# Kernel optimization log

Measured on AMD Instinct MI355X. Metric: run time of the kernel, lower is better.

Reference implementation:

```python
import jax, jax.numpy as jnp
import numpy as np

N_NODES = 50000
N_EDGES = 800000
F_IN = 128
HID = 128
N_CLASSES = 16
N_GRAPHS = 64


def _glorot(key, shape):
    fan_in, fan_out = shape[0], shape[1]
    lim = (6.0 / (fan_in + fan_out)) ** 0.5
    return jax.random.uniform(key, shape, jnp.float32, -lim, lim)


def setup_inputs() -> dict:
    key = jax.random.key(0)
    ks = jax.random.split(key, 12)
    x = jax.random.normal(ks[0], (N_NODES, F_IN), jnp.float32)
    edge_index = jax.random.randint(ks[1], (2, N_EDGES), 0, N_NODES, jnp.int64)
    batch = jnp.sort(jax.random.randint(ks[2], (N_NODES,), 0, N_GRAPHS, jnp.int64))
    W0 = _glorot(ks[3], (F_IN, HID)); b0 = jnp.zeros((HID,), jnp.float32)
    W1 = _glorot(ks[4], (HID, HID)); b1 = jnp.zeros((HID,), jnp.float32)
    W2 = _glorot(ks[5], (HID, HID)); b2 = jnp.zeros((HID,), jnp.float32)
    Wc = _glorot(ks[6], (HID, N_CLASSES)); bc = jnp.zeros((N_CLASSES,), jnp.float32)
    return {"x": x, "edge_index": edge_index, "batch": batch,
            "W0": W0, "b0": b0, "W1": W1, "b1": b1, "W2": W2, "b2": b2,
            "Wc": Wc, "bc": bc}


def _gcn_prep(edge_index, n_nodes):
    # add self-loops, compute symmetric normalization coefficients
    loop = jnp.arange(n_nodes, dtype=edge_index.dtype)
    src = jnp.concatenate([edge_index[0], loop])
    dst = jnp.concatenate([edge_index[1], loop])
    deg = jax.ops.segment_sum(jnp.ones_like(dst, jnp.float32), dst, num_segments=n_nodes)
    dinv = deg ** -0.5  # deg >= 1 due to self-loops
    norm = dinv[src] * dinv[dst]  # [E+N]
    return src, dst, norm


def _gcn_layer(h, W, b, src, dst, norm, n_nodes):
    h = h @ W                                   # [N, out]
    msg = h[src] * norm[:, None]                # gather + scale [E+N, out]
    out = jax.ops.segment_sum(msg, dst, num_segments=n_nodes)  # scatter-add
    return out + b


def reference(x, edge_index, batch, W0, b0, W1, b1, W2, b2, Wc, bc):
    n = x.shape[0]
    src, dst, norm = _gcn_prep(edge_index, n)
    h = _gcn_layer(x, W0, b0, src, dst, norm, n)
    h = jax.nn.relu(h)  # dropout is identity in eval mode
    h = _gcn_layer(h, W1, b1, src, dst, norm, n)
    h = jax.nn.relu(h)
    h = _gcn_layer(h, W2, b2, src, dst, norm, n)
    # scatter-mean pooling over batch ids
    sums = jax.ops.segment_sum(h, batch, num_segments=N_GRAPHS)        # [G, HID]
    cnts = jax.ops.segment_sum(jnp.ones((n,), jnp.float32), batch, num_segments=N_GRAPHS)
    pooled = sums / jnp.maximum(cnts, 1.0)[:, None]
    return pooled @ Wc + bc  # [G, N_CLASSES]
```

## Files before the change

### kernel.cpp

```cpp
#include <hip/hip_runtime.h>
#include <hip/hip_bf16.h>
#include <hip/hip_fp16.h>

#define HID 128
#define NCLS 16
#define NGRAPH 64
#define CHUNK 1024

using bf16x8 = __attribute__((ext_vector_type(8))) short;
using f32x4  = __attribute__((ext_vector_type(4))) float;

__device__ __forceinline__ unsigned int f2bf(float f) {
    unsigned int u = __float_as_uint(f);
    return (u + 0x7FFFu + ((u >> 16) & 1u)) >> 16;
}
__device__ __forceinline__ float bf2f_lo(unsigned int u) { return __uint_as_float(u << 16); }
__device__ __forceinline__ float bf2f_hi(unsigned int u) { return __uint_as_float(u & 0xFFFF0000u); }

__global__ __launch_bounds__(256) void k_init(int* counts, float* pooled, float* cnt, int n) {
    int i = blockIdx.x * 256 + threadIdx.x;
    if (i < n) counts[i] = 0;
    if (i < NGRAPH * HID) pooled[i] = 0.0f;
    if (i < NGRAPH) cnt[i] = 0.0f;
}

__global__ __launch_bounds__(256) void k_hist(const int* __restrict__ dst,
                                              int* counts, int* rank, int e) {
    int i = blockIdx.x * 256 + threadIdx.x;
    if (i < e) rank[i] = atomicAdd(&counts[dst[i]], 1);
}

__global__ __launch_bounds__(256) void k_dinv(const int* __restrict__ counts,
                                              float* dinv, int n) {
    int i = blockIdx.x * 256 + threadIdx.x;
    if (i < n) dinv[i] = rsqrtf((float)(counts[i] + 1));
}

__global__ __launch_bounds__(256) void k_chunksum(const int* __restrict__ counts,
                                                  int* csum, int n) {
    __shared__ int sdata[256];
    int b = blockIdx.x, t = threadIdx.x;
    int base = b * CHUNK + t * 4;
    int s = 0;
    #pragma unroll
    for (int j = 0; j < 4; ++j) { int i = base + j; if (i < n) s += counts[i]; }
    sdata[t] = s; __syncthreads();
    for (int off = 128; off > 0; off >>= 1) {
        if (t < off) sdata[t] += sdata[t + off];
        __syncthreads();
    }
    if (t == 0) csum[b] = sdata[0];
}

__global__ void k_scanchunks(const int* __restrict__ csum, int* coff, int nb) {
    if (blockIdx.x == 0 && threadIdx.x == 0) {
        int run = 0;
        for (int b = 0; b < nb; ++b) { coff[b] = run; run += csum[b]; }
    }
}

__global__ __launch_bounds__(256) void k_rowptr(const int* __restrict__ counts,
                                                const int* __restrict__ coff,
                                                int* rowptr, int n, int e) {
    __shared__ int sincl[256];
    int b = blockIdx.x, t = threadIdx.x;
    int base = b * CHUNK + t * 4;
    int v[4]; int s = 0;
    #pragma unroll
    for (int j = 0; j < 4; ++j) { int i = base + j; v[j] = (i < n) ? counts[i] : 0; s += v[j]; }
    sincl[t] = s; __syncthreads();
    for (int off = 1; off < 256; off <<= 1) {
        int x = sincl[t];
        int y = (t >= off) ? sincl[t - off] : 0;
        __syncthreads();
        sincl[t] = x + y;
        __syncthreads();
    }
    int run = coff[b] + sincl[t] - s;
    #pragma unroll
    for (int j = 0; j < 4; ++j) {
        int i = base + j;
        if (i < n) { rowptr[i] = run; run += v[j]; }
    }
    if (b == 0 && t == 0) rowptr[n] = e;
}

__global__ __launch_bounds__(256) void k_fill(const int* __restrict__ src,
                                              const int* __restrict__ dst,
                                              const int* __restrict__ rank,
                                              const float* __restrict__ dinv,
                                              const int* __restrict__ rowptr,
                                              unsigned int* __restrict__ epk, int e) {
    int i = blockIdx.x * 256 + threadIdx.x;
    if (i >= e) return;
    int s = src[i], d = dst[i];
    int pos = rowptr[d] + rank[i];
    __half h = __float2half(dinv[s] * dinv[d]);
    unsigned int hu = (unsigned int)__half_as_ushort(h);
    epk[pos] = (unsigned int)s | (hu << 16);
}

__global__ __launch_bounds__(256) void k_wprep(const float* __restrict__ W0,
                                               const float* __restrict__ W1,
                                               const float* __restrict__ W2,
                                               unsigned short* __restrict__ Wt) {
    int tid = blockIdx.x * 256 + threadIdx.x;
    if (tid >= 3 * HID * HID) return;
    int m = tid >> 14;
    int r = tid & 16383;
    int c = r >> 7, k = r & 127;
    const float* W = (m == 0) ? W0 : (m == 1) ? W1 : W2;
    Wt[tid] = (unsigned short)f2bf(W[k * HID + c]);
}

__global__ __launch_bounds__(256) void k_gemm_f32(const float* __restrict__ H,
                                                  const unsigned short* __restrict__ Wt,
                                                  unsigned short* __restrict__ Tb16, int n) {
    __shared__ char ldsA[64 * 256];
    int t = threadIdx.x;
    int cg = t & 31;
    int rg = t >> 5;
    int row0 = blockIdx.x * 64;

    #pragma unroll
    for (int i = 0; i < 8; ++i) {
        int lr = rg + i * 8;
        int r = row0 + lr;
        float4 v = make_float4(0.f, 0.f, 0.f, 0.f);
        if (r < n) v = ((const float4*)H)[(size_t)r * 32 + cg];
        uint2 pk;
        pk.x = f2bf(v.x) | (f2bf(v.y) << 16);
        pk.y = f2bf(v.z) | (f2bf(v.w) << 16);
        int byte = lr * 256 + cg * 8;
        *(uint2*)(ldsA + (byte ^ ((lr & 7) << 4))) = pk;
    }
    __syncthreads();

    int lane = t & 63;
    int w = t >> 6;
    int rsub = lane & 15;
    int kg = lane >> 4;
    int rowIdx = w * 16 + rsub;
    int abase = rowIdx * 256 + kg * 16;
    int aswz = (rowIdx & 7) << 4;

    f32x4 acc[8];
    #pragma unroll
    for (int nt = 0; nt < 8; ++nt) acc[nt] = (f32x4)(0.f);

    #pragma unroll
    for (int kk = 0; kk < 4; ++kk) {
        bf16x8 a = *(const bf16x8*)(ldsA + ((abase + kk * 64) ^ aswz));
        int k0 = kk * 32 + kg * 8;
        #pragma unroll
        for (int nt = 0; nt < 8; ++nt) {
            int col = nt * 16 + rsub;
            bf16x8 b = *(const bf16x8*)(Wt + col * 128 + k0);
            acc[nt] = __builtin_amdgcn_mfma_f32_16x16x32_bf16(a, b, acc[nt], 0, 0, 0);
        }
    }

    #pragma unroll
    for (int nt = 0; nt < 8; ++nt) {
        #pragma unroll
        for (int j = 0; j < 4; ++j) {
            int row = row0 + w * 16 + kg * 4 + j;
            int col = nt * 16 + rsub;
            if (row < n) Tb16[(size_t)row * 128 + col] = (unsigned short)f2bf(acc[nt][j]);
        }
    }
}

__global__ __launch_bounds__(256) void k_gemm_bf16(const unsigned short* __restrict__ Hb,
                                                   const unsigned short* __restrict__ Wt,
                                                   unsigned short* __restrict__ Tb16, int n) {
    __shared__ char ldsA[64 * 256];
    int t = threadIdx.x;
    int row0 = blockIdx.x * 64;
    int c16 = t & 15;
    int rbase = t >> 4;

    #pragma unroll
    for (int i = 0; i < 4; ++i) {
        int lr = rbase + i * 16;
        int r = row0 + lr;
        uint4 v = make_uint4(0u, 0u, 0u, 0u);
        if (r < n) v = *(const uint4*)(Hb + (size_t)r * 128 + c16 * 8);
        int byte = lr * 256 + c16 * 16;
        *(uint4*)(ldsA + (byte ^ ((lr & 7) << 4))) = v;
    }
    __syncthreads();

    int lane = t & 63;
    int w = t >> 6;
    int rsub = lane & 15;
    int kg = lane >> 4;
    int rowIdx = w * 16 + rsub;
    int abase = rowIdx * 256 + kg * 16;
    int aswz = (rowIdx & 7) << 4;

    f32x4 acc[8];
    #pragma unroll
    for (int nt = 0; nt < 8; ++nt) acc[nt] = (f32x4)(0.f);

    #pragma unroll
    for (int kk = 0; kk < 4; ++kk) {
        bf16x8 a = *(const bf16x8*)(ldsA + ((abase + kk * 64) ^ aswz));
        int k0 = kk * 32 + kg * 8;
        #pragma unroll
        for (int nt = 0; nt < 8; ++nt) {
            int col = nt * 16 + rsub;
            bf16x8 b = *(const bf16x8*)(Wt + col * 128 + k0);
            acc[nt] = __builtin_amdgcn_mfma_f32_16x16x32_bf16(a, b, acc[nt], 0, 0, 0);
        }
    }

    #pragma unroll
    for (int nt = 0; nt < 8; ++nt) {
        #pragma unroll
        for (int j = 0; j < 4; ++j) {
            int row = row0 + w * 16 + kg * 4 + j;
            int col = nt * 16 + rsub;
            if (row < n) Tb16[(size_t)row * 128 + col] = (unsigned short)f2bf(acc[nt][j]);
        }
    }
}

__global__ __launch_bounds__(256) void k_agg(const unsigned int* __restrict__ Tb,
                                             unsigned int* __restrict__ outB,
                                             float* __restrict__ outF,
                                             const int* __restrict__ rowptr,
                                             const unsigned int* __restrict__ epk,
                                             const float* __restrict__ dinv,
                                             const float* __restrict__ bias,
                                             int n, int mode) {
    int wid = (blockIdx.x * 256 + threadIdx.x) >> 6;
    int lane = threadIdx.x & 63;
    if (wid >= n) return;
    float di = dinv[wid];
    float2 b2 = ((const float2*)bias)[lane];
    unsigned int us = Tb[(size_t)wid * 64 + lane];
    float sn = di * di;
    float2 acc;
    acc.x = fmaf(bf2f_lo(us), sn, b2.x);
    acc.y = fmaf(bf2f_hi(us), sn, b2.y);
    int start = rowptr[wid];
    int deg = rowptr[wid + 1] - start;

    for (int j0 = 0; j0 < deg; j0 += 64) {
        int myj = j0 + lane;
        unsigned int rec = 0;
        if (myj < deg) rec = epk[start + myj];
        int m = min(64, deg - j0);
        int jj = 0;
        for (; jj + 16 <= m; jj += 16) {
            unsigned int rr[16], uu[16];
            #pragma unroll
            for (int k = 0; k < 16; ++k) rr[k] = (unsigned int)__shfl((int)rec, jj + k);
            #pragma unroll
            for (int k = 0; k < 16; ++k) uu[k] = Tb[(size_t)(rr[k] & 0xFFFFu) * 64 + lane];
            #pragma unroll
            for (int k = 0; k < 16; ++k) {
                float wk = __half2float(__ushort_as_half((unsigned short)(rr[k] >> 16)));
                acc.x = fmaf(wk, bf2f_lo(uu[k]), acc.x);
                acc.y = fmaf(wk, bf2f_hi(uu[k]), acc.y);
            }
        }
        for (; jj + 4 <= m; jj += 4) {
            unsigned int rr[4], uu[4];
            #pragma unroll
            for (int k = 0; k < 4; ++k) rr[k] = (unsigned int)__shfl((int)rec, jj + k);
            #pragma unroll
            for (int k = 0; k < 4; ++k) uu[k] = Tb[(size_t)(rr[k] & 0xFFFFu) * 64 + lane];
            #pragma unroll
            for (int k = 0; k < 4; ++k) {
                float wk = __half2float(__ushort_as_half((unsigned short)(rr[k] >> 16)));
                acc.x = fmaf(wk, bf2f_lo(uu[k]), acc.x);
                acc.y = fmaf(wk, bf2f_hi(uu[k]), acc.y);
            }
        }
        for (; jj < m; ++jj) {
            unsigned int rj = (unsigned int)__shfl((int)rec, jj);
            unsigned int u = Tb[(size_t)(rj & 0xFFFFu) * 64 + lane];
            float wj = __half2float(__ushort_as_half((unsigned short)(rj >> 16)));
            acc.x = fmaf(wj, bf2f_lo(u), acc.x);
            acc.y = fmaf(wj, bf2f_hi(u), acc.y);
        }
    }

    if (mode == 0) {
        float rx = fmaxf(acc.x, 0.f), ry = fmaxf(acc.y, 0.f);
        outB[(size_t)wid * 64 + lane] = f2bf(rx) | (f2bf(ry) << 16);
    } else {
        ((float2*)outF)[(size_t)wid * 64 + lane] = acc;
    }
}

__global__ __launch_bounds__(256) void k_pool(const float* __restrict__ H,
                                              const int* __restrict__ batch,
                                              float* pooled, float* cnt, int n) {
    int gw = (blockIdx.x * 256 + threadIdx.x) >> 6;
    int lane = threadIdx.x & 63;
    int n0 = gw * 32;
    if (n0 >= n) return;
    int n1 = min(n0 + 32, n);
    const float2* H2 = (const float2*)H;
    int gprev = batch[n0];
    float2 acc = make_float2(0.f, 0.f);
    float runc = 0.f;
    for (int i = n0; i < n1; ++i) {
        int g = batch[i];
        if (g != gprev) {
            atomicAdd(&pooled[gprev * HID + 2 * lane], acc.x);
            atomicAdd(&pooled[gprev * HID + 2 * lane + 1], acc.y);
            if (lane == 0) atomicAdd(&cnt[gprev], runc);
            acc = make_float2(0.f, 0.f); runc = 0.f; gprev = g;
        }
        float2 v = H2[(size_t)i * 64 + lane];
        acc.x += v.x; acc.y += v.y; runc += 1.f;
    }
    atomicAdd(&pooled[gprev * HID + 2 * lane], acc.x);
    atomicAdd(&pooled[gprev * HID + 2 * lane + 1], acc.y);
    if (lane == 0) atomicAdd(&cnt[gprev], runc);
}

__global__ __launch_bounds__(256) void k_head(const float* __restrict__ pooled,
                                              const float* __restrict__ cnt,
                                              const float* __restrict__ Wc,
                                              const float* __restrict__ bc,
                                              float* __restrict__ out) {
    int idx = blockIdx.x * 256 + threadIdx.x;
    if (idx >= NGRAPH * NCLS) return;
    int g = idx >> 4, c = idx & 15;
    float inv = 1.0f / fmaxf(cnt[g], 1.0f);
    float s = 0.f;
    for (int k = 0; k < HID; ++k)
        s = fmaf(pooled[g * HID + k], Wc[k * NCLS + c], s);
    out[idx] = s * inv + bc[c];
}

extern "C" void kernel_launch(void* const* d_in, const int* in_sizes, int n_in,
                              void* d_out, int out_size, void* d_ws, size_t ws_size,
                              hipStream_t stream) {
    const float* x    = (const float*)d_in[0];
    const int*   ei   = (const int*)d_in[1];
    const int*   batch= (const int*)d_in[2];
    const float* W0   = (const float*)d_in[3];
    const float* b0   = (const float*)d_in[4];
    const float* W1   = (const float*)d_in[5];
    const float* b1   = (const float*)d_in[6];
    const float* W2   = (const float*)d_in[7];
    const float* b2   = (const float*)d_in[8];
    const float* Wc   = (const float*)d_in[9];
    const float* bc   = (const float*)d_in[10];
    float* out = (float*)d_out;

    const int N = in_sizes[0] / HID;
    const int E = in_sizes[1] / 2;
    const int* src = ei;
    const int* dst = ei + E;

    char* p = (char*)d_ws;
    auto alloc = [&](size_t bytes) { void* r = (void*)p; p += (bytes + 255) & ~(size_t)255; return r; };
    int*   counts = (int*)alloc((size_t)N * 4);
    float* dinv   = (float*)alloc((size_t)N * 4);
    int*   rank   = (int*)alloc((size_t)E * 4);
    int*   csum   = (int*)alloc(256 * 4);
    int*   coff   = (int*)alloc(256 * 4);
    int*   rowptr = (int*)alloc((size_t)(N + 1) * 4);
    unsigned int* epk = (unsigned int*)alloc((size_t)E * 4);
    float* pooled = (float*)alloc((size_t)NGRAPH * HID * 4);
    float* cnt    = (float*)alloc((size_t)NGRAPH * 4);
    unsigned short* Tb16 = (unsigned short*)alloc((size_t)N * HID * 2);
    unsigned short* Hb16 = (unsigned short*)alloc((size_t)N * HID * 2);
    float* bufF   = (float*)alloc((size_t)N * HID * 4);
    unsigned short* Wt = (unsigned short*)alloc((size_t)3 * HID * HID * 2);

    const int NB = (N + CHUNK - 1) / CHUNK;

    k_init<<<(N + 255) / 256, 256, 0, stream>>>(counts, pooled, cnt, N);
    k_hist<<<(E + 255) / 256, 256, 0, stream>>>(dst, counts, rank, E);
    k_dinv<<<(N + 255) / 256, 256, 0, stream>>>(counts, dinv, N);
    k_chunksum<<<NB, 256, 0, stream>>>(counts, csum, N);
    k_scanchunks<<<1, 64, 0, stream>>>(csum, coff, NB);
    k_rowptr<<<NB, 256, 0, stream>>>(counts, coff, rowptr, N, E);
    k_fill<<<(E + 255) / 256, 256, 0, stream>>>(src, dst, rank, dinv, rowptr, epk, E);
    k_wprep<<<(3 * HID * HID + 255) / 256, 256, 0, stream>>>(W0, W1, W2, Wt);

    const int gemm_grid = (N + 63) / 64;
    const int agg_grid  = ((size_t)N * 64 + 255) / 256;

    k_gemm_f32<<<gemm_grid, 256, 0, stream>>>(x, Wt, Tb16, N);
    k_agg<<<agg_grid, 256, 0, stream>>>((const unsigned int*)Tb16, (unsigned int*)Hb16, nullptr,
                                        rowptr, epk, dinv, b0, N, 0);
    k_gemm_bf16<<<gemm_grid, 256, 0, stream>>>(Hb16, Wt + 16384, Tb16, N);
    k_agg<<<agg_grid, 256, 0, stream>>>((const unsigned int*)Tb16, (unsigned int*)Hb16, nullptr,
                                        rowptr, epk, dinv, b1, N, 0);
    k_gemm_bf16<<<gemm_grid, 256, 0, stream>>>(Hb16, Wt + 32768, Tb16, N);
    k_agg<<<agg_grid, 256, 0, stream>>>((const unsigned int*)Tb16, nullptr, bufF,
                                        rowptr, epk, dinv, b2, N, 1);

    const int pool_waves = (N + 31) / 32;
    k_pool<<<(pool_waves * 64 + 255) / 256, 256, 0, stream>>>(bufF, batch, pooled, cnt, N);
    k_head<<<(NGRAPH * NCLS + 255) / 256, 256, 0, stream>>>(pooled, cnt, Wc, bc, out);
}
```

Measured before the change: 264.5 us.

## Split feature tables into column halves for cache-resident aggregation; fold prep kernels

The bf16 feature tables are now stored as two 64-column halves. Aggregation runs as two passes per layer, each touching a 6.4 MB half table, so the gathered working set is more likely to stay in L2 or last-level cache. Within each pass a wave splits its edges between two 32-lane groups and reduces them with a cross-half shuffle. The dinv, scan-chunks and weight-prep kernels are folded into init, rowptr and fill, removing several launches. In exchange the edge list and rowptr are read twice per layer, and each aggregation launch does less work per node.

```diff
diff --git a/kernel.cpp b/kernel.cpp
--- a/kernel.cpp
+++ b/kernel.cpp
@@ -17,23 +17,28 @@
 __device__ __forceinline__ float bf2f_lo(unsigned int u) { return __uint_as_float(u << 16); }
 __device__ __forceinline__ float bf2f_hi(unsigned int u) { return __uint_as_float(u & 0xFFFF0000u); }
 
-__global__ __launch_bounds__(256) void k_init(int* counts, float* pooled, float* cnt, int n) {
+__global__ __launch_bounds__(256) void k_init(int* counts, float* pooled, float* cnt,
+                                              const float* __restrict__ W0,
+                                              const float* __restrict__ W1,
+                                              const float* __restrict__ W2,
+                                              unsigned short* __restrict__ Wt, int n) {
     int i = blockIdx.x * 256 + threadIdx.x;
     if (i < n) counts[i] = 0;
     if (i < NGRAPH * HID) pooled[i] = 0.0f;
     if (i < NGRAPH) cnt[i] = 0.0f;
+    if (i < 3 * HID * HID) {
+        int m = i >> 14;
+        int r = i & 16383;
+        int c = r >> 7, k = r & 127;
+        const float* W = (m == 0) ? W0 : (m == 1) ? W1 : W2;
+        Wt[i] = (unsigned short)f2bf(W[k * HID + c]);
+    }
 }
 
 __global__ __launch_bounds__(256) void k_hist(const int* __restrict__ dst,
                                               int* counts, int* rank, int e) {
     int i = blockIdx.x * 256 + threadIdx.x;
     if (i < e) rank[i] = atomicAdd(&counts[dst[i]], 1);
-}
-
-__global__ __launch_bounds__(256) void k_dinv(const int* __restrict__ counts,
-                                              float* dinv, int n) {
-    int i = blockIdx.x * 256 + threadIdx.x;
-    if (i < n) dinv[i] = rsqrtf((float)(counts[i] + 1));
 }
 
 __global__ __launch_bounds__(256) void k_chunksum(const int* __restrict__ counts,
@@ -52,18 +57,18 @@
     if (t == 0) csum[b] = sdata[0];
 }
 
-__global__ void k_scanchunks(const int* __restrict__ csum, int* coff, int nb) {
-    if (blockIdx.x == 0 && threadIdx.x == 0) {
-        int run = 0;
-        for (int b = 0; b < nb; ++b) { coff[b] = run; run += csum[b]; }
-    }
-}
-
 __global__ __launch_bounds__(256) void k_rowptr(const int* __restrict__ counts,
-                                                const int* __restrict__ coff,
+                                                const int* __restrict__ csum,
                                                 int* rowptr, int n, int e) {
     __shared__ int sincl[256];
+    __shared__ int s_coff;
     int b = blockIdx.x, t = threadIdx.x;
+    if (t < 64) {
+        int v = (t < b) ? csum[t] : 0;
+        #pragma unroll
+        for (int off = 32; off > 0; off >>= 1) v += __shfl_xor(v, off);
+        if (t == 0) s_coff = v;
+    }
     int base = b * CHUNK + t * 4;
     int v[4]; int s = 0;
     #pragma unroll
@@ -76,7 +81,7 @@
         sincl[t] = x + y;
         __syncthreads();
     }
-    int run = coff[b] + sincl[t] - s;
+    int run = s_coff + sincl[t] - s;
     #pragma unroll
     for (int j = 0; j < 4; ++j) {
         int i = base + j;
@@ -88,34 +93,23 @@
 __global__ __launch_bounds__(256) void k_fill(const int* __restrict__ src,
                                               const int* __restrict__ dst,
                                               const int* __restrict__ rank,
-                                              const float* __restrict__ dinv,
+                                              const int* __restrict__ counts,
                                               const int* __restrict__ rowptr,
                                               unsigned int* __restrict__ epk, int e) {
     int i = blockIdx.x * 256 + threadIdx.x;
     if (i >= e) return;
     int s = src[i], d = dst[i];
     int pos = rowptr[d] + rank[i];
-    __half h = __float2half(dinv[s] * dinv[d]);
+    float norm = rsqrtf((float)(counts[s] + 1)) * rsqrtf((float)(counts[d] + 1));
+    __half h = __float2half(norm);
     unsigned int hu = (unsigned int)__half_as_ushort(h);
     epk[pos] = (unsigned int)s | (hu << 16);
 }
 
-__global__ __launch_bounds__(256) void k_wprep(const float* __restrict__ W0,
-                                               const float* __restrict__ W1,
-                                               const float* __restrict__ W2,
-                                               unsigned short* __restrict__ Wt) {
-    int tid = blockIdx.x * 256 + threadIdx.x;
-    if (tid >= 3 * HID * HID) return;
-    int m = tid >> 14;
-    int r = tid & 16383;
-    int c = r >> 7, k = r & 127;
-    const float* W = (m == 0) ? W0 : (m == 1) ? W1 : W2;
-    Wt[tid] = (unsigned short)f2bf(W[k * HID + c]);
-}
-
 __global__ __launch_bounds__(256) void k_gemm_f32(const float* __restrict__ H,
                                                   const unsigned short* __restrict__ Wt,
-                                                  unsigned short* __restrict__ Tb16, int n) {
+                                                  unsigned short* __restrict__ Tlo,
+                                                  unsigned short* __restrict__ Thi, int n) {
     __shared__ char ldsA[64 * 256];
     int t = threadIdx.x;
     int cg = t & 31;
@@ -162,18 +156,21 @@
 
     #pragma unroll
     for (int nt = 0; nt < 8; ++nt) {
+        unsigned short* Tb = (nt < 4) ? Tlo : Thi;
         #pragma unroll
         for (int j = 0; j < 4; ++j) {
             int row = row0 + w * 16 + kg * 4 + j;
-            int col = nt * 16 + rsub;
-            if (row < n) Tb16[(size_t)row * 128 + col] = (unsigned short)f2bf(acc[nt][j]);
-        }
-    }
-}
-
-__global__ __launch_bounds__(256) void k_gemm_bf16(const unsigned short* __restrict__ Hb,
+            int col = (nt * 16 + rsub) & 63;
+            if (row < n) Tb[(size_t)row * 64 + col] = (unsigned short)f2bf(acc[nt][j]);
+        }
+    }
+}
+
+__global__ __launch_bounds__(256) void k_gemm_bf16(const unsigned short* __restrict__ Hlo,
+                                                   const unsigned short* __restrict__ Hhi,
                                                    const unsigned short* __restrict__ Wt,
-                                                   unsigned short* __restrict__ Tb16, int n) {
+                                                   unsigned short* __restrict__ Tlo,
+                                                   unsigned short* __restrict__ Thi, int n) {
     __shared__ char ldsA[64 * 256];
     int t = threadIdx.x;
     int row0 = blockIdx.x * 64;
@@ -184,8 +181,9 @@
     for (int i = 0; i < 4; ++i) {
         int lr = rbase + i * 16;
         int r = row0 + lr;
+        const unsigned short* Hb = (c16 < 8) ? Hlo : Hhi;
         uint4 v = make_uint4(0u, 0u, 0u, 0u);
-        if (r < n) v = *(const uint4*)(Hb + (size_t)r * 128 + c16 * 8);
+        if (r < n) v = *(const uint4*)(Hb + (size_t)r * 64 + (c16 & 7) * 8);
         int byte = lr * 256 + c16 * 16;
         *(uint4*)(ldsA + (byte ^ ((lr & 7) << 4))) = v;
     }
@@ -217,82 +215,80 @@
 
     #pragma unroll
     for (int nt = 0; nt < 8; ++nt) {
+        unsigned short* Tb = (nt < 4) ? Tlo : Thi;
         #pragma unroll
         for (int j = 0; j < 4; ++j) {
             int row = row0 + w * 16 + kg * 4 + j;
-            int col = nt * 16 + rsub;
-            if (row < n) Tb16[(size_t)row * 128 + col] = (unsigned short)f2bf(acc[nt][j]);
-        }
-    }
-}
-
-__global__ __launch_bounds__(256) void k_agg(const unsigned int* __restrict__ Tb,
-                                             unsigned int* __restrict__ outB,
-                                             float* __restrict__ outF,
-                                             const int* __restrict__ rowptr,
-                                             const unsigned int* __restrict__ epk,
-                                             const float* __restrict__ dinv,
-                                             const float* __restrict__ bias,
-                                             int n, int mode) {
+            int col = (nt * 16 + rsub) & 63;
+            if (row < n) Tb[(size_t)row * 64 + col] = (unsigned short)f2bf(acc[nt][j]);
+        }
+    }
+}
+
+__global__ __launch_bounds__(256) void k_agg_h(const unsigned int* __restrict__ TbH,
+                                               unsigned int* __restrict__ outB,
+                                               float* __restrict__ outF,
+                                               const int* __restrict__ rowptr,
+                                               const unsigned int* __restrict__ epk,
+                                               const float* __restrict__ biasH,
+                                               int n, int mode, int hoff) {
     int wid = (blockIdx.x * 256 + threadIdx.x) >> 6;
     int lane = threadIdx.x & 63;
     if (wid >= n) return;
-    float di = dinv[wid];
-    float2 b2 = ((const float2*)bias)[lane];
-    unsigned int us = Tb[(size_t)wid * 64 + lane];
-    float sn = di * di;
-    float2 acc;
-    acc.x = fmaf(bf2f_lo(us), sn, b2.x);
-    acc.y = fmaf(bf2f_hi(us), sn, b2.y);
+    int p = lane & 31;
+    int g = lane >> 5;
     int start = rowptr[wid];
     int deg = rowptr[wid + 1] - start;
 
+    float2 acc = make_float2(0.f, 0.f);
+    if (g == 0) {
+        float sn = 1.0f / (float)(deg + 1);
+        unsigned int us = TbH[(size_t)wid * 32 + p];
+        float2 b2 = ((const float2*)biasH)[p];
+        acc.x = fmaf(bf2f_lo(us), sn, b2.x);
+        acc.y = fmaf(bf2f_hi(us), sn, b2.y);
+    }
+
+    int gbase = g * 32;
     for (int j0 = 0; j0 < deg; j0 += 64) {
-        int myj = j0 + lane;
+        int myj = j0 + 2 * p + g;
         unsigned int rec = 0;
         if (myj < deg) rec = epk[start + myj];
-        int m = min(64, deg - j0);
+        int rem = deg - j0 - g;
+        int mg = min(32, (rem + 1) >> 1);
         int jj = 0;
-        for (; jj + 16 <= m; jj += 16) {
-            unsigned int rr[16], uu[16];
+        for (; jj + 8 <= mg; jj += 8) {
+            unsigned int rr[8], uu[8];
             #pragma unroll
-            for (int k = 0; k < 16; ++k) rr[k] = (unsigned int)__shfl((int)rec, jj + k);
+            for (int k = 0; k < 8; ++k) rr[k] = (unsigned int)__shfl((int)rec, gbase + jj + k);
             #pragma unroll
-            for (int k = 0; k < 16; ++k) uu[k] = Tb[(size_t)(rr[k] & 0xFFFFu) * 64 + lane];
+            for (int k = 0; k < 8; ++k) uu[k] = TbH[(size_t)(rr[k] & 0xFFFFu) * 32 + p];
             #pragma unroll
-            for (int k = 0; k < 16; ++k) {
+            for (int k = 0; k < 8; ++k) {
                 float wk = __half2float(__ushort_as_half((unsigned short)(rr[k] >> 16)));
                 acc.x = fmaf(wk, bf2f_lo(uu[k]), acc.x);
                 acc.y = fmaf(wk, bf2f_hi(uu[k]), acc.y);
             }
         }
-        for (; jj + 4 <= m; jj += 4) {
-            unsigned int rr[4], uu[4];
-            #pragma unroll
-            for (int k = 0; k < 4; ++k) rr[k] = (unsigned int)__shfl((int)rec, jj + k);
-            #pragma unroll
-            for (int k = 0; k < 4; ++k) uu[k] = Tb[(size_t)(rr[k] & 0xFFFFu) * 64 + lane];
-            #pragma unroll
-            for (int k = 0; k < 4; ++k) {
-                float wk = __half2float(__ushort_as_half((unsigned short)(rr[k] >> 16)));
-                acc.x = fmaf(wk, bf2f_lo(uu[k]), acc.x);
-                acc.y = fmaf(wk, bf2f_hi(uu[k]), acc.y);
-            }
-        }
-        for (; jj < m; ++jj) {
-            unsigned int rj = (unsigned int)__shfl((int)rec, jj);
-            unsigned int u = Tb[(size_t)(rj & 0xFFFFu) * 64 + lane];
+        for (; jj < mg; ++jj) {
+            unsigned int rj = (unsigned int)__shfl((int)rec, gbase + jj);
+            unsigned int u = TbH[(size_t)(rj & 0xFFFFu) * 32 + p];
             float wj = __half2float(__ushort_as_half((unsigned short)(rj >> 16)));
             acc.x = fmaf(wj, bf2f_lo(u), acc.x);
             acc.y = fmaf(wj, bf2f_hi(u), acc.y);
         }
     }
 
-    if (mode == 0) {
-        float rx = fmaxf(acc.x, 0.f), ry = fmaxf(acc.y, 0.f);
-        outB[(size_t)wid * 64 + lane] = f2bf(rx) | (f2bf(ry) << 16);
-    } else {
-        ((float2*)outF)[(size_t)wid * 64 + lane] = acc;
+    acc.x += __shfl_xor(acc.x, 32);
+    acc.y += __shfl_xor(acc.y, 32);
+
+    if (g == 0) {
+        if (mode == 0) {
+            float rx = fmaxf(acc.x, 0.f), ry = fmaxf(acc.y, 0.f);
+            outB[(size_t)wid * 32 + p] = f2bf(rx) | (f2bf(ry) << 16);
+        } else {
+            ((float2*)outF)[(size_t)wid * 64 + hoff + p] = acc;
+        }
     }
 }
 
@@ -363,42 +359,45 @@
     char* p = (char*)d_ws;
     auto alloc = [&](size_t bytes) { void* r = (void*)p; p += (bytes + 255) & ~(size_t)255; return r; };
     int*   counts = (int*)alloc((size_t)N * 4);
-    float* dinv   = (float*)alloc((size_t)N * 4);
     int*   rank   = (int*)alloc((size_t)E * 4);
     int*   csum   = (int*)alloc(256 * 4);
-    int*   coff   = (int*)alloc(256 * 4);
     int*   rowptr = (int*)alloc((size_t)(N + 1) * 4);
     unsigned int* epk = (unsigned int*)alloc((size_t)E * 4);
     float* pooled = (float*)alloc((size_t)NGRAPH * HID * 4);
     float* cnt    = (float*)alloc((size_t)NGRAPH * 4);
-    unsigned short* Tb16 = (unsigned short*)alloc((size_t)N * HID * 2);
-    unsigned short* Hb16 = (unsigned short*)alloc((size_t)N * HID * 2);
+    unsigned short* Tlo = (unsigned short*)alloc((size_t)N * 64 * 2);
+    unsigned short* Thi = (unsigned short*)alloc((size_t)N * 64 * 2);
+    unsigned short* Hlo = (unsigned short*)alloc((size_t)N * 64 * 2);
+    unsigned short* Hhi = (unsigned short*)alloc((size_t)N * 64 * 2);
     float* bufF   = (float*)alloc((size_t)N * HID * 4);
     unsigned short* Wt = (unsigned short*)alloc((size_t)3 * HID * HID * 2);
 
     const int NB = (N + CHUNK - 1) / CHUNK;
 
-    k_init<<<(N + 255) / 256, 256, 0, stream>>>(counts, pooled, cnt, N);
+    k_init<<<(N + 255) / 256, 256, 0, stream>>>(counts, pooled, cnt, W0, W1, W2, Wt, N);
     k_hist<<<(E + 255) / 256, 256, 0, stream>>>(dst, counts, rank, E);
-    k_dinv<<<(N + 255) / 256, 256, 0, stream>>>(counts, dinv, N);
     k_chunksum<<<NB, 256, 0, stream>>>(counts, csum, N);
-    k_scanchunks<<<1, 64, 0, stream>>>(csum, coff, NB);
-    k_rowptr<<<NB, 256, 0, stream>>>(counts, coff, rowptr, N, E);
-    k_fill<<<(E + 255) / 256, 256, 0, stream>>>(src, dst, rank, dinv, rowptr, epk, E);
-    k_wprep<<<(3 * HID * HID + 255) / 256, 256, 0, stream>>>(W0, W1, W2, Wt);
+    k_rowptr<<<NB, 256, 0, stream>>>(counts, csum, rowptr, N, E);
+    k_fill<<<(E + 255) / 256, 256, 0, stream>>>(src, dst, rank, counts, rowptr, epk, E);
 
     const int gemm_grid = (N + 63) / 64;
     const int agg_grid  = ((size_t)N * 64 + 255) / 256;
 
-    k_gemm_f32<<<gemm_grid, 256, 0, stream>>>(x, Wt, Tb16, N);
-    k_agg<<<agg_grid, 256, 0, stream>>>((const unsigned int*)Tb16, (unsigned int*)Hb16, nullptr,
-                                        rowptr, epk, dinv, b0, N, 0);
-    k_gemm_bf16<<<gemm_grid, 256, 0, stream>>>(Hb16, Wt + 16384, Tb16, N);
-    k_agg<<<agg_grid, 256, 0, stream>>>((const unsigned int*)Tb16, (unsigned int*)Hb16, nullptr,
-                                        rowptr, epk, dinv, b1, N, 0);
-    k_gemm_bf16<<<gemm_grid, 256, 0, stream>>>(Hb16, Wt + 32768, Tb16, N);
-    k_agg<<<agg_grid, 256, 0, stream>>>((const unsigned int*)Tb16, nullptr, bufF,
-                                        rowptr, epk, dinv, b2, N, 1);
+    k_gemm_f32<<<gemm_grid, 256, 0, stream>>>(x, Wt, Tlo, Thi, N);
+    k_agg_h<<<agg_grid, 256, 0, stream>>>((const unsigned int*)Tlo, (unsigned int*)Hlo, nullptr,
+                                          rowptr, epk, b0, N, 0, 0);
+    k_agg_h<<<agg_grid, 256, 0, stream>>>((const unsigned int*)Thi, (unsigned int*)Hhi, nullptr,
+                                          rowptr, epk, b0 + 64, N, 0, 32);
+    k_gemm_bf16<<<gemm_grid, 256, 0, stream>>>(Hlo, Hhi, Wt + 16384, Tlo, Thi, N);
+    k_agg_h<<<agg_grid, 256, 0, stream>>>((const unsigned int*)Tlo, (unsigned int*)Hlo, nullptr,
+                                          rowptr, epk, b1, N, 0, 0);
+    k_agg_h<<<agg_grid, 256, 0, stream>>>((const unsigned int*)Thi, (unsigned int*)Hhi, nullptr,
+                                          rowptr, epk, b1 + 64, N, 0, 32);
+    k_gemm_bf16<<<gemm_grid, 256, 0, stream>>>(Hlo, Hhi, Wt + 32768, Tlo, Thi, N);
+    k_agg_h<<<agg_grid, 256, 0, stream>>>((const unsigned int*)Tlo, nullptr, bufF,
+                                          rowptr, epk, b2, N, 1, 0);
+    k_agg_h<<<agg_grid, 256, 0, stream>>>((const unsigned int*)Thi, nullptr, bufF,
+                                          rowptr, epk, b2 + 64, N, 1, 32);
 
     const int pool_waves = (N + 31) / 32;
     k_pool<<<(pool_waves * 64 + 255) / 256, 256, 0, stream>>>(bufF, batch, pooled, cnt, N);
```

New measurement: 322.7 us. +22.0%, slower.

## Fold classifier weights into last GCN layer to aggregate 16-wide features

Applied to the files above, without the earlier changes.

Because the last layer has no nonlinearity and mean-pooling is linear, W2 and Wc are premultiplied (W2·Wc, b2·Wc+bc), so the final GEMM, aggregation and pooling run on 16 columns instead of 128. This removes most of the gather traffic of the third aggregation and the fp32 128-wide intermediate buffer. The change also folds the degree-inverse computation into the fill and aggregation kernels, merges the chunk-offset scan into the rowptr kernel, and moves weight conversion into the init kernel, cutting several launches. The combined W2·Wc product is rounded to bf16, which changes rounding slightly.

```diff
diff --git a/kernel.cpp b/kernel.cpp
--- a/kernel.cpp
+++ b/kernel.cpp
@@ -17,23 +17,50 @@
 __device__ __forceinline__ float bf2f_lo(unsigned int u) { return __uint_as_float(u << 16); }
 __device__ __forceinline__ float bf2f_hi(unsigned int u) { return __uint_as_float(u & 0xFFFF0000u); }
 
-__global__ __launch_bounds__(256) void k_init(int* counts, float* pooled, float* cnt, int n) {
+__global__ __launch_bounds__(256) void k_init(int* counts, float* pooled, float* cnt,
+                                              const float* __restrict__ W0,
+                                              const float* __restrict__ W1,
+                                              unsigned short* __restrict__ Wt, int n) {
     int i = blockIdx.x * 256 + threadIdx.x;
     if (i < n) counts[i] = 0;
-    if (i < NGRAPH * HID) pooled[i] = 0.0f;
+    if (i < NGRAPH * NCLS) pooled[i] = 0.0f;
     if (i < NGRAPH) cnt[i] = 0.0f;
+    if (i < 2 * HID * HID) {
+        int m = i >> 14;
+        int r = i & 16383;
+        int c = r >> 7, k = r & 127;
+        const float* W = (m == 0) ? W0 : W1;
+        Wt[i] = (unsigned short)f2bf(W[k * HID + c]);
+    }
+}
+
+__global__ __launch_bounds__(256) void k_wc(const float* __restrict__ W2,
+                                            const float* __restrict__ Wc,
+                                            const float* __restrict__ b2,
+                                            const float* __restrict__ bcin,
+                                            unsigned short* __restrict__ Wt2c,
+                                            float* __restrict__ bc2) {
+    int tid = blockIdx.x * 256 + threadIdx.x;
+    if (tid < HID * NCLS) {
+        int k = tid >> 4, c = tid & 15;
+        float s = 0.f;
+        #pragma unroll 8
+        for (int j = 0; j < HID; ++j)
+            s = fmaf(W2[k * HID + j], Wc[j * NCLS + c], s);
+        Wt2c[c * 128 + k] = (unsigned short)f2bf(s);
+    }
+    if (tid < NCLS) {
+        float s = 0.f;
+        for (int j = 0; j < HID; ++j)
+            s = fmaf(b2[j], Wc[j * NCLS + tid], s);
+        bc2[tid] = s + bcin[tid];
+    }
 }
 
 __global__ __launch_bounds__(256) void k_hist(const int* __restrict__ dst,
                                               int* counts, int* rank, int e) {
     int i = blockIdx.x * 256 + threadIdx.x;
     if (i < e) rank[i] = atomicAdd(&counts[dst[i]], 1);
-}
-
-__global__ __launch_bounds__(256) void k_dinv(const int* __restrict__ counts,
-                                              float* dinv, int n) {
-    int i = blockIdx.x * 256 + threadIdx.x;
-    if (i < n) dinv[i] = rsqrtf((float)(counts[i] + 1));
 }
 
 __global__ __launch_bounds__(256) void k_chunksum(const int* __restrict__ counts,
@@ -52,18 +79,18 @@
     if (t == 0) csum[b] = sdata[0];
 }
 
-__global__ void k_scanchunks(const int* __restrict__ csum, int* coff, int nb) {
-    if (blockIdx.x == 0 && threadIdx.x == 0) {
-        int run = 0;
-        for (int b = 0; b < nb; ++b) { coff[b] = run; run += csum[b]; }
-    }
-}
-
 __global__ __launch_bounds__(256) void k_rowptr(const int* __restrict__ counts,
-                                                const int* __restrict__ coff,
+                                                const int* __restrict__ csum,
                                                 int* rowptr, int n, int e) {
     __shared__ int sincl[256];
+    __shared__ int s_coff;
     int b = blockIdx.x, t = threadIdx.x;
+    if (t < 64) {
+        int v = (t < b) ? csum[t] : 0;
+        #pragma unroll
+        for (int off = 32; off > 0; off >>= 1) v += __shfl_xor(v, off);
+        if (t == 0) s_coff = v;
+    }
     int base = b * CHUNK + t * 4;
     int v[4]; int s = 0;
     #pragma unroll
@@ -76,7 +103,7 @@
         sincl[t] = x + y;
         __syncthreads();
     }
-    int run = coff[b] + sincl[t] - s;
+    int run = s_coff + sincl[t] - s;
     #pragma unroll
     for (int j = 0; j < 4; ++j) {
         int i = base + j;
@@ -88,29 +115,17 @@
 __global__ __launch_bounds__(256) void k_fill(const int* __restrict__ src,
                                               const int* __restrict__ dst,
                                               const int* __restrict__ rank,
-                                              const float* __restrict__ dinv,
+                                              const int* __restrict__ counts,
                                               const int* __restrict__ rowptr,
                                               unsigned int* __restrict__ epk, int e) {
     int i = blockIdx.x * 256 + threadIdx.x;
     if (i >= e) return;
     int s = src[i], d = dst[i];
     int pos = rowptr[d] + rank[i];
-    __half h = __float2half(dinv[s] * dinv[d]);
+    float norm = rsqrtf((float)(counts[s] + 1)) * rsqrtf((float)(counts[d] + 1));
+    __half h = __float2half(norm);
     unsigned int hu = (unsigned int)__half_as_ushort(h);
     epk[pos] = (unsigned int)s | (hu << 16);
-}
-
-__global__ __launch_bounds__(256) void k_wprep(const float* __restrict__ W0,
-                                               const float* __restrict__ W1,
-                                               const float* __restrict__ W2,
-                                               unsigned short* __restrict__ Wt) {
-    int tid = blockIdx.x * 256 + threadIdx.x;
-    if (tid >= 3 * HID * HID) return;
-    int m = tid >> 14;
-    int r = tid & 16383;
-    int c = r >> 7, k = r & 127;
-    const float* W = (m == 0) ? W0 : (m == 1) ? W1 : W2;
-    Wt[tid] = (unsigned short)f2bf(W[k * HID + c]);
 }
 
 __global__ __launch_bounds__(256) void k_gemm_f32(const float* __restrict__ H,
@@ -226,26 +241,66 @@
     }
 }
 
+__global__ __launch_bounds__(256) void k_gemm16(const unsigned short* __restrict__ Hb,
+                                                const unsigned short* __restrict__ Wt2c,
+                                                float* __restrict__ T16, int n) {
+    __shared__ char ldsA[64 * 256];
+    int t = threadIdx.x;
+    int row0 = blockIdx.x * 64;
+    int c16 = t & 15;
+    int rbase = t >> 4;
+
+    #pragma unroll
+    for (int i = 0; i < 4; ++i) {
+        int lr = rbase + i * 16;
+        int r = row0 + lr;
+        uint4 v = make_uint4(0u, 0u, 0u, 0u);
+        if (r < n) v = *(const uint4*)(Hb + (size_t)r * 128 + c16 * 8);
+        int byte = lr * 256 + c16 * 16;
+        *(uint4*)(ldsA + (byte ^ ((lr & 7) << 4))) = v;
+    }
+    __syncthreads();
+
+    int lane = t & 63;
+    int w = t >> 6;
+    int rsub = lane & 15;
+    int kg = lane >> 4;
+    int rowIdx = w * 16 + rsub;
+    int abase = rowIdx * 256 + kg * 16;
+    int aswz = (rowIdx & 7) << 4;
+
+    f32x4 acc = (f32x4)(0.f);
+    #pragma unroll
+    for (int kk = 0; kk < 4; ++kk) {
+        bf16x8 a = *(const bf16x8*)(ldsA + ((abase + kk * 64) ^ aswz));
+        int k0 = kk * 32 + kg * 8;
+        bf16x8 b = *(const bf16x8*)(Wt2c + rsub * 128 + k0);
+        acc = __builtin_amdgcn_mfma_f32_16x16x32_bf16(a, b, acc, 0, 0, 0);
+    }
+
+    #pragma unroll
+    for (int j = 0; j < 4; ++j) {
+        int row = row0 + w * 16 + kg * 4 + j;
+        if (row < n) T16[(size_t)row * 16 + rsub] = acc[j];
+    }
+}
+
 __global__ __launch_bounds__(256) void k_agg(const unsigned int* __restrict__ Tb,
                                              unsigned int* __restrict__ outB,
-                                             float* __restrict__ outF,
                                              const int* __restrict__ rowptr,
                                              const unsigned int* __restrict__ epk,
-                                             const float* __restrict__ dinv,
-                                             const float* __restrict__ bias,
-                                             int n, int mode) {
+                                             const float* __restrict__ bias, int n) {
     int wid = (blockIdx.x * 256 + threadIdx.x) >> 6;
     int lane = threadIdx.x & 63;
     if (wid >= n) return;
-    float di = dinv[wid];
     float2 b2 = ((const float2*)bias)[lane];
     unsigned int us = Tb[(size_t)wid * 64 + lane];
-    float sn = di * di;
+    int start = rowptr[wid];
+    int deg = rowptr[wid + 1] - start;
+    float sn = 1.0f / (float)(deg + 1);
     float2 acc;
     acc.x = fmaf(bf2f_lo(us), sn, b2.x);
     acc.y = fmaf(bf2f_hi(us), sn, b2.y);
-    int start = rowptr[wid];
-    int deg = rowptr[wid + 1] - start;
 
     for (int j0 = 0; j0 < deg; j0 += 64) {
         int myj = j0 + lane;
@@ -288,55 +343,99 @@
         }
     }
 
-    if (mode == 0) {
-        float rx = fmaxf(acc.x, 0.f), ry = fmaxf(acc.y, 0.f);
-        outB[(size_t)wid * 64 + lane] = f2bf(rx) | (f2bf(ry) << 16);
-    } else {
-        ((float2*)outF)[(size_t)wid * 64 + lane] = acc;
-    }
-}
-
-__global__ __launch_bounds__(256) void k_pool(const float* __restrict__ H,
-                                              const int* __restrict__ batch,
-                                              float* pooled, float* cnt, int n) {
+    float rx = fmaxf(acc.x, 0.f), ry = fmaxf(acc.y, 0.f);
+    outB[(size_t)wid * 64 + lane] = f2bf(rx) | (f2bf(ry) << 16);
+}
+
+__global__ __launch_bounds__(256) void k_agg16(const float* __restrict__ T16,
+                                               float* __restrict__ G16,
+                                               const int* __restrict__ rowptr,
+                                               const unsigned int* __restrict__ epk, int n) {
+    int wid = (blockIdx.x * 256 + threadIdx.x) >> 6;
+    int lane = threadIdx.x & 63;
+    if (wid >= n) return;
+    int p = lane & 15;
+    int q = lane >> 4;
+    int start = rowptr[wid];
+    int deg = rowptr[wid + 1] - start;
+
+    float acc = 0.f;
+    if (q == 0) {
+        float sn = 1.0f / (float)(deg + 1);
+        acc = T16[(size_t)wid * 16 + p] * sn;
+    }
+
+    for (int j0 = 0; j0 < deg; j0 += 64) {
+        int myj = j0 + lane;
+        unsigned int rec = 0;
+        if (myj < deg) rec = epk[start + myj];
+        int m = min(64, deg - j0);
+        int mg = (m - q + 3) >> 2;
+        int jj = 0;
+        for (; jj + 8 <= mg; jj += 8) {
+            unsigned int rr[8]; float uu[8];
+            #pragma unroll
+            for (int k = 0; k < 8; ++k) rr[k] = (unsigned int)__shfl((int)rec, 4 * (jj + k) + q);
+            #pragma unroll
+            for (int k = 0; k < 8; ++k) uu[k] = T16[(size_t)(rr[k] & 0xFFFFu) * 16 + p];
+            #pragma unroll
+            for (int k = 0; k < 8; ++k) {
+                float wk = __half2float(__ushort_as_half((unsigned short)(rr[k] >> 16)));
+                acc = fmaf(wk, uu[k], acc);
+            }
+        }
+        for (; jj < mg; ++jj) {
+            unsigned int rj = (unsigned int)__shfl((int)rec, 4 * jj + q);
+            float u = T16[(size_t)(rj & 0xFFFFu) * 16 + p];
+            float wj = __half2float(__ushort_as_half((unsigned short)(rj >> 16)));
+            acc = fmaf(wj, u, acc);
+        }
+    }
+
+    acc += __shfl_xor(acc, 16);
+    acc += __shfl_xor(acc, 32);
+
+    if (q == 0) G16[(size_t)wid * 16 + p] = acc;
+}
+
+__global__ __launch_bounds__(256) void k_pool16(const float* __restrict__ G16,
+                                                const int* __restrict__ batch,
+                                                float* pooled, float* cnt, int n) {
     int gw = (blockIdx.x * 256 + threadIdx.x) >> 6;
     int lane = threadIdx.x & 63;
-    int n0 = gw * 32;
+    int p = lane & 15;
+    int q = lane >> 4;
+    int n0 = gw * 64;
     if (n0 >= n) return;
-    int n1 = min(n0 + 32, n);
-    const float2* H2 = (const float2*)H;
-    int gprev = batch[n0];
-    float2 acc = make_float2(0.f, 0.f);
+    int n1 = min(n0 + 64, n);
+    int i0 = n0 + q;
+    if (i0 >= n1) return;
+    int gprev = batch[i0];
+    float acc = 0.f;
     float runc = 0.f;
-    for (int i = n0; i < n1; ++i) {
+    for (int i = i0; i < n1; i += 4) {
         int g = batch[i];
         if (g != gprev) {
-            atomicAdd(&pooled[gprev * HID + 2 * lane], acc.x);
-            atomicAdd(&pooled[gprev * HID + 2 * lane + 1], acc.y);
-            if (lane == 0) atomicAdd(&cnt[gprev], runc);
-            acc = make_float2(0.f, 0.f); runc = 0.f; gprev = g;
-        }
-        float2 v = H2[(size_t)i * 64 + lane];
-        acc.x += v.x; acc.y += v.y; runc += 1.f;
-    }
-    atomicAdd(&pooled[gprev * HID + 2 * lane], acc.x);
-    atomicAdd(&pooled[gprev * HID + 2 * lane + 1], acc.y);
-    if (lane == 0) atomicAdd(&cnt[gprev], runc);
-}
-
-__global__ __launch_bounds__(256) void k_head(const float* __restrict__ pooled,
-                                              const float* __restrict__ cnt,
-                                              const float* __restrict__ Wc,
-                                              const float* __restrict__ bc,
-                                              float* __restrict__ out) {
+            atomicAdd(&pooled[gprev * NCLS + p], acc);
+            if (p == 0) atomicAdd(&cnt[gprev], runc);
+            acc = 0.f; runc = 0.f; gprev = g;
+        }
+        acc += G16[(size_t)i * 16 + p];
+        runc += 1.f;
+    }
+    atomicAdd(&pooled[gprev * NCLS + p], acc);
+    if (p == 0) atomicAdd(&cnt[gprev], runc);
+}
+
+__global__ __launch_bounds__(256) void k_head16(const float* __restrict__ pooled,
+                                                const float* __restrict__ cnt,
+                                                const float* __restrict__ bc2,
+                                                float* __restrict__ out) {
     int idx = blockIdx.x * 256 + threadIdx.x;
     if (idx >= NGRAPH * NCLS) return;
     int g = idx >> 4, c = idx & 15;
     float inv = 1.0f / fmaxf(cnt[g], 1.0f);
-    float s = 0.f;
-    for (int k = 0; k < HID; ++k)
-        s = fmaf(pooled[g * HID + k], Wc[k * NCLS + c], s);
-    out[idx] = s * inv + bc[c];
+    out[idx] = pooled[idx] * inv + bc2[c];
 }
 
 extern "C" void kernel_launch(void* const* d_in, const int* in_sizes, int n_in,
@@ -363,44 +462,42 @@
     char* p = (char*)d_ws;
     auto alloc = [&](size_t bytes) { void* r = (void*)p; p += (bytes + 255) & ~(size_t)255; return r; };
     int*   counts = (int*)alloc((size_t)N * 4);
-    float* dinv   = (float*)alloc((size_t)N * 4);
     int*   rank   = (int*)alloc((size_t)E * 4);
     int*   csum   = (int*)alloc(256 * 4);
-    int*   coff   = (int*)alloc(256 * 4);
     int*   rowptr = (int*)alloc((size_t)(N + 1) * 4);
     unsigned int* epk = (unsigned int*)alloc((size_t)E * 4);
-    float* pooled = (float*)alloc((size_t)NGRAPH * HID * 4);
+    float* pooled = (float*)alloc((size_t)NGRAPH * NCLS * 4);
     float* cnt    = (float*)alloc((size_t)NGRAPH * 4);
     unsigned short* Tb16 = (unsigned short*)alloc((size_t)N * HID * 2);
     unsigned short* Hb16 = (unsigned short*)alloc((size_t)N * HID * 2);
-    float* bufF   = (float*)alloc((size_t)N * HID * 4);
-    unsigned short* Wt = (unsigned short*)alloc((size_t)3 * HID * HID * 2);
+    float* T16    = (float*)alloc((size_t)N * NCLS * 4);
+    float* G16    = (float*)alloc((size_t)N * NCLS * 4);
+    unsigned short* Wt   = (unsigned short*)alloc((size_t)2 * HID * HID * 2);
+    unsigned short* Wt2c = (unsigned short*)alloc((size_t)NCLS * 128 * 2);
+    float* bc2    = (float*)alloc(NCLS * 4);
 
     const int NB = (N + CHUNK - 1) / CHUNK;
 
-    k_init<<<(N + 255) / 256, 256, 0, stream>>>(counts, pooled, cnt, N);
+    k_init<<<(N + 255) / 256, 256, 0, stream>>>(counts, pooled, cnt, W0, W1, Wt, N);
     k_hist<<<(E + 255) / 256, 256, 0, stream>>>(dst, counts, rank, E);
-    k_dinv<<<(N + 255) / 256, 256, 0, stream>>>(counts, dinv, N);
     k_chunksum<<<NB, 256, 0, stream>>>(counts, csum, N);
-    k_scanchunks<<<1, 64, 0, stream>>>(csum, coff, NB);
-    k_rowptr<<<NB, 256, 0, stream>>>(counts, coff, rowptr, N, E);
-    k_fill<<<(E + 255) / 256, 256, 0, stream>>>(src, dst, rank, dinv, rowptr, epk, E);
-    k_wprep<<<(3 * HID * HID + 255) / 256, 256, 0, stream>>>(W0, W1, W2, Wt);
+    k_rowptr<<<NB, 256, 0, stream>>>(counts, csum, rowptr, N, E);
+    k_fill<<<(E + 255) / 256, 256, 0, stream>>>(src, dst, rank, counts, rowptr, epk, E);
+    k_wc<<<(HID * NCLS + 255) / 256, 256, 0, stream>>>(W2, Wc, b2, bc, Wt2c, bc2);
 
     const int gemm_grid = (N + 63) / 64;
     const int agg_grid  = ((size_t)N * 64 + 255) / 256;
 
     k_gemm_f32<<<gemm_grid, 256, 0, stream>>>(x, Wt, Tb16, N);
-    k_agg<<<agg_grid, 256, 0, stream>>>((const unsigned int*)Tb16, (unsigned int*)Hb16, nullptr,
-                                        rowptr, epk, dinv, b0, N, 0);
+    k_agg<<<agg_grid, 256, 0, stream>>>((const unsigned int*)Tb16, (unsigned int*)Hb16,
+                                        rowptr, epk, b0, N);
     k_gemm_bf16<<<gemm_grid, 256, 0, stream>>>(Hb16, Wt + 16384, Tb16, N);
-    k_agg<<<agg_grid, 256, 0, stream>>>((const unsigned int*)Tb16, (unsigned int*)Hb16, nullptr,
-                                        rowptr, epk, dinv, b1, N, 0);
-    k_gemm_bf16<<<gemm_grid, 256, 0, stream>>>(Hb16, Wt + 32768, Tb16, N);
-    k_agg<<<agg_grid, 256, 0, stream>>>((const unsigned int*)Tb16, nullptr, bufF,
-                                        rowptr, epk, dinv, b2, N, 1);
-
-    const int pool_waves = (N + 31) / 32;
-    k_pool<<<(pool_waves * 64 + 255) / 256, 256, 0, stream>>>(bufF, batch, pooled, cnt, N);
-    k_head<<<(NGRAPH * NCLS + 255) / 256, 256, 0, stream>>>(pooled, cnt, Wc, bc, out);
-}
+    k_agg<<<agg_grid, 256, 0, stream>>>((const unsigned int*)Tb16, (unsigned int*)Hb16,
+                                        rowptr, epk, b1, N);
+    k_gemm16<<<gemm_grid, 256, 0, stream>>>(Hb16, Wt2c, T16, N);
+    k_agg16<<<agg_grid, 256, 0, stream>>>(T16, G16, rowptr, epk, N);
+
+    const int pool_blocks = (((N + 63) / 64) * 64 + 255) / 256;
+    k_pool16<<<pool_blocks, 256, 0, stream>>>(G16, batch, pooled, cnt, N);
+    k_head16<<<(NGRAPH * NCLS + 255) / 256, 256, 0, stream>>>(pooled, cnt, bc2, out);
+}
```

Result: faster. 236.8 us (-10.5%).
